# Optimization experiments

Hardware: AMD Instinct MI355X
Metric: run time of the kernel (lower is better)

The kernel has to match this reference:

```python
import jax, jax.numpy as jnp
import numpy as np

S_CONST = float(np.log(9.0))   # self.s = log(9)
K = 1.0                        # soft_sign sharpness (config.k)
RHO = 1.0
ALPHA0 = 0.01
BETA0 = 0.1
DECAY = 0.99


def soft_sign(x, k=K):
    # E2Efold soft sign: sigmoid(2*k*x)
    return jax.nn.sigmoid(2.0 * k * x)


def constraint_matrix(x):
    # x: [B, L, 4] -> m: [B, L, L]; pairing constraint AU+CG+UG outer products,
    # symmetrized, with |i-j|<=3 band zeroed (diags mask in torch version).
    base_a, base_u, base_c, base_g = x[..., 0], x[..., 1], x[..., 2], x[..., 3]

    def sym_outer(p, q):
        m = p[:, :, None] * q[:, None, :]
        return m + jnp.swapaxes(m, -1, -2)

    m = sym_outer(base_a, base_u) + sym_outer(base_c, base_g) + sym_outer(base_u, base_g)
    L = x.shape[1]
    i = jnp.arange(L)
    band = jnp.abs(i[:, None] - i[None, :]) <= 3  # [L, L] bool
    return jnp.where(band, jnp.zeros((), m.dtype), m)


def contact_a(a_hat, m):
    a = a_hat * a_hat
    a = (a + jnp.swapaxes(a, -1, -2)) * 0.5
    return a * m


def setup_inputs() -> dict:
    key = jax.random.key(0)
    k1, k2 = jax.random.split(key)
    B, L = 16, 512
    u = jax.random.normal(k1, (B, L, L), jnp.float32) * 2.0
    x = jax.random.uniform(k2, (B, L, 4), jnp.float32)
    return {"u": u, "x": x, "timesteps": 20}


def reference(u, x, timesteps):
    m = constraint_matrix(x)
    u = soft_sign(u - S_CONST) * u
    a_hat = jax.nn.sigmoid(u) * jax.lax.stop_gradient(soft_sign(u - S_CONST))
    a = contact_a(a_hat, m)
    lmbd = jax.lax.stop_gradient(jax.nn.relu(jnp.sum(a, -1) - 1.0))

    # per-step decayed learning rates: step t uses alpha0*decay^t (for grad step)
    # and alpha0*decay^(t+1) for the soft-threshold (torch decays alpha in between)
    t_idx = jnp.arange(timesteps, dtype=jnp.float32)
    alphas = ALPHA0 * DECAY ** t_idx
    betas = BETA0 * DECAY ** t_idx

    def step(carry, ab):
        lmbd, a, a_hat = carry
        alpha, beta = ab
        grad_a = -u / 2.0 + (lmbd * soft_sign(jnp.sum(a, -1) - 1.0))[..., None]
        grad = a_hat * m * (grad_a + jnp.swapaxes(grad_a, -1, -2))
        a_hat_new = a_hat - alpha * grad
        a_hat_new = jax.nn.relu(jnp.abs(a_hat_new) - RHO * alpha * DECAY)
        a_hat_new = jnp.clip(a_hat_new, -1.0, 1.0)
        a_new = contact_a(a_hat_new, m)
        lmbd_new = lmbd + beta * jax.nn.relu(jnp.sum(a_new, -1) - 1.0)
        return (lmbd_new, a_new, a_hat_new), a_new

    _, a_stack = jax.lax.scan(step, (lmbd, a, a_hat), (alphas, betas))
    return a_stack  # [timesteps, B, L, L] == a_t_list[1:]
```

## Files before the change

kernel.cpp:

```cpp
#include <hip/hip_runtime.h>
#include <math.h>

#define BB 16
#define LL 512
#define TS 20
#define TT 64
#define NT (LL / TT)
#define NPAIR (NT * (NT + 1) / 2)
#define NUNIT 32
#define NBLK (BB * NUNIT)
#define BLL (BB * LL * LL)
#define NROW (BB * LL)
#define RSPSTEP (BB * NT * LL)

#define S_CONST 2.19722457733621938f

__device__ __forceinline__ float sgm(float v) { return 1.0f / (1.0f + __expf(-v)); }
__device__ __forceinline__ float ahat_of(float up) {
  return sgm(up) * sgm(2.0f * (up - S_CONST));
}

__device__ __forceinline__ void st_agent(float* p, float v) {
  __hip_atomic_store(p, v, __ATOMIC_RELAXED, __HIP_MEMORY_SCOPE_AGENT);
}
__device__ __forceinline__ float ld_agent(const float* p) {
  return __hip_atomic_load(p, __ATOMIC_RELAXED, __HIP_MEMORY_SCOPE_AGENT);
}

__device__ __forceinline__ void bar_lds() {
  asm volatile("s_waitcnt lgkmcnt(0)" ::: "memory");
  __builtin_amdgcn_s_barrier();
  asm volatile("" ::: "memory");
}

__device__ __forceinline__ void decode_unit(int p, int& RI, int& RJ, bool& dg) {
  if (p < 28) {
    int base = 0, i = 0;
    while (p >= base + (NT - 1 - i)) { base += NT - 1 - i; ++i; }
    RI = i;
    RJ = i + 1 + (p - base);
    dg = false;
  } else {
    int g = p - 28;
    RI = 2 * g;
    RJ = 2 * g + 1;
    dg = true;
  }
}

__global__ __launch_bounds__(256, 2) void k_fused(const float* __restrict__ u,
                                                  const float* __restrict__ x,
                                                  float* __restrict__ rsp,
                                                  float* __restrict__ out) {
  __shared__ float t1[TT][TT + 1];
  __shared__ float t2[TT][TT + 1];
  __shared__ float colp1[16][TT];
  __shared__ float colp2[16][TT];
  __shared__ float rp1[TT];
  __shared__ float rp2[TT];
  __shared__ float xr[2][TT][4];
  __shared__ float xt[2][TT][4];
  __shared__ float cI[TT];
  __shared__ float cJ[TT];

  int b = blockIdx.x / NUNIT;
  int p = blockIdx.x % NUNIT;
  int RI, RJ;
  bool dg;
  decode_unit(p, RI, RJ, dg);
  int C1 = dg ? RI : RJ;
  int C2 = dg ? RJ : RI;

  int tid = threadIdx.x;
  int tx = tid & 15, ty = tid >> 4;

  if (tid < 128) {
    int which = tid >> 6;
    int r = tid & 63;
    int gi = (which ? RJ : RI) * TT + r;
    const float* xp = x + ((b * LL) + gi) * 4;
    float A = xp[0], U = xp[1], C = xp[2], G = xp[3];
    xr[which][r][0] = A; xr[which][r][1] = U; xr[which][r][2] = C; xr[which][r][3] = G;
    xt[which][r][0] = U; xt[which][r][1] = A + G; xt[which][r][2] = G; xt[which][r][3] = C + U;
  }

  int lrow = 0;
  if (tid < 128) {
    int which = tid >> 6;
    int r = tid & 63;
    lrow = (which ? RJ : RI) * TT + r;
  }
  float lmbd = 0.0f;

  float av1[4][4], av2[4][4];
  float wv1[4][4], wv2[4][4];
  float mv1[4][4], mv2[4][4];

  __syncthreads();

#pragma unroll
  for (int k = 0; k < 4; ++k) {
    int r = ty + 16 * k;
    {
      int i = RI * TT + r;
      int off = (b * LL + i) * LL + C1 * TT + 4 * tx;
      float4 u4 = *reinterpret_cast<const float4*>(u + off);
      float uu[4] = {u4.x, u4.y, u4.z, u4.w};
#pragma unroll
      for (int q = 0; q < 4; ++q) {
        float up = sgm(2.0f * (uu[q] - S_CONST)) * uu[q];
        t1[r][4 * tx + q] = up;
        av1[k][q] = ahat_of(up);
      }
    }
    {
      int i = RJ * TT + r;
      int off = (b * LL + i) * LL + C2 * TT + 4 * tx;
      float4 u4 = *reinterpret_cast<const float4*>(u + off);
      float uu[4] = {u4.x, u4.y, u4.z, u4.w};
#pragma unroll
      for (int q = 0; q < 4; ++q) {
        float up = sgm(2.0f * (uu[q] - S_CONST)) * uu[q];
        t2[r][4 * tx + q] = up;
        av2[k][q] = ahat_of(up);
      }
    }
  }
  __syncthreads();

  {
    float (*T1)[TT + 1] = dg ? t1 : t2;
    float (*T2)[TT + 1] = dg ? t2 : t1;
    float (*xc1)[4] = dg ? xt[0] : xt[1];
    float (*xc2)[4] = dg ? xt[1] : xt[0];
    float* rsp0 = rsp;

#pragma unroll
    for (int k = 0; k < 4; ++k) {
      int r = ty + 16 * k;
      {
        int i = RI * TT + r;
        float rs = 0.0f;
#pragma unroll
        for (int q = 0; q < 4; ++q) {
          int c = 4 * tx + q;
          int j = C1 * TT + c;
          float upT = T1[c][r];
          wv1[k][q] = -0.5f * (t1[r][c] + upT);
          int d = i - j; d = d < 0 ? -d : d;
          float mm = (d <= 3) ? 0.0f
                              : xr[0][r][0] * xc1[c][0] + xr[0][r][1] * xc1[c][1] +
                                    xr[0][r][2] * xc1[c][2] + xr[0][r][3] * xc1[c][3];
          mv1[k][q] = mm;
          float aT = ahat_of(upT);
          float a = av1[k][q];
          rs += 0.5f * (a * a + aT * aT) * mm;
        }
        rs += __shfl_xor(rs, 1); rs += __shfl_xor(rs, 2);
        rs += __shfl_xor(rs, 4); rs += __shfl_xor(rs, 8);
        if (tx == 0) st_agent(&rsp0[(b * NT + C1) * LL + i], rs + 1.0f);
      }
      {
        int i = RJ * TT + r;
        float rs = 0.0f;
#pragma unroll
        for (int q = 0; q < 4; ++q) {
          int c = 4 * tx + q;
          int j = C2 * TT + c;
          float upT = T2[c][r];
          wv2[k][q] = -0.5f * (t2[r][c] + upT);
          int d = i - j; d = d < 0 ? -d : d;
          float mm = (d <= 3) ? 0.0f
                              : xr[1][r][0] * xc2[c][0] + xr[1][r][1] * xc2[c][1] +
                                    xr[1][r][2] * xc2[c][2] + xr[1][r][3] * xc2[c][3];
          mv2[k][q] = mm;
          float aT = ahat_of(upT);
          float a = av2[k][q];
          rs += 0.5f * (a * a + aT * aT) * mm;
        }
        rs += __shfl_xor(rs, 1); rs += __shfl_xor(rs, 2);
        rs += __shfl_xor(rs, 4); rs += __shfl_xor(rs, 8);
        if (tx == 0) st_agent(&rsp0[(b * NT + C2) * LL + i], rs + 1.0f);
      }
    }
  }

  float (*T1)[TT + 1] = dg ? t1 : t2;
  float (*T2)[TT + 1] = dg ? t2 : t1;

  float alpha = 0.01f;
  float beta_prev = 0.0f;

  for (int t = 0; t < TS; ++t) {
    if (tid < 128) {
      const float* rp = rsp + (size_t)t * RSPSTEP + b * NT * LL + lrow;
      float v0, v1, v2, v3, v4, v5, v6, v7;
      for (;;) {
        v0 = ld_agent(rp + 0 * LL);
        v1 = ld_agent(rp + 1 * LL);
        v2 = ld_agent(rp + 2 * LL);
        v3 = ld_agent(rp + 3 * LL);
        v4 = ld_agent(rp + 4 * LL);
        v5 = ld_agent(rp + 5 * LL);
        v6 = ld_agent(rp + 6 * LL);
        v7 = ld_agent(rp + 7 * LL);
        bool ok = (v0 != 0.0f) & (v1 != 0.0f) & (v2 != 0.0f) & (v3 != 0.0f) &
                  (v4 != 0.0f) & (v5 != 0.0f) & (v6 != 0.0f) & (v7 != 0.0f);
        if (__all(ok)) break;
        __builtin_amdgcn_s_sleep(2);
        asm volatile("" ::: "memory");
      }
      float rsv = ((v0 + v1) + (v2 + v3)) + ((v4 + v5) + (v6 + v7));
      float dv = rsv - 9.0f;
      float rel = dv > 0.0f ? dv : 0.0f;
      lmbd = (t == 0) ? rel : lmbd + beta_prev * rel;
      float cv = lmbd * sgm(2.0f * dv);
      if (tid >= 64) cJ[tid & 63] = cv; else cI[tid] = cv;
    } else if (t > 0) {
      int tid2 = tid - 128;
      int tx2 = tid2 & 15, ty2 = tid2 >> 4;
      float* op = out + (size_t)(t - 1) * BLL;
#pragma unroll
      for (int k = 0; k < 8; ++k) {
        int r = ty2 + 8 * k;
        {
          int off = (b * LL + RI * TT + r) * LL + C1 * TT + 4 * tx2;
          float res[4];
#pragma unroll
          for (int q = 0; q < 4; ++q) {
            int c = 4 * tx2 + q;
            res[q] = t1[r][c] + T1[c][r];
          }
          *reinterpret_cast<float4*>(op + off) = make_float4(res[0], res[1], res[2], res[3]);
        }
        {
          int off = (b * LL + RJ * TT + r) * LL + C2 * TT + 4 * tx2;
          float res[4];
#pragma unroll
          for (int q = 0; q < 4; ++q) {
            int c = 4 * tx2 + q;
            res[q] = t2[r][c] + T2[c][r];
          }
          *reinterpret_cast<float4*>(op + off) = make_float4(res[0], res[1], res[2], res[3]);
        }
      }
    }
    bar_lds();

    float thr = alpha * 0.99f;
    float* cc1 = dg ? cI : cJ;
    float* cc2 = dg ? cJ : cI;

    float cp1[4] = {0.f, 0.f, 0.f, 0.f};
    float cp2[4] = {0.f, 0.f, 0.f, 0.f};
#pragma unroll
    for (int k = 0; k < 4; ++k) {
      int r = ty + 16 * k;
      {
        float ci = cI[r];
        float rsv = 0.0f;
#pragma unroll
        for (int q = 0; q < 4; ++q) {
          int c = 4 * tx + q;
          float a = av1[k][q];
          float g = a * mv1[k][q] * (wv1[k][q] + ci + cc1[c]);
          float an = a - alpha * g;
          an = fabsf(an) - thr;
          an = an > 0.0f ? an : 0.0f;
          an = an < 1.0f ? an : 1.0f;
          av1[k][q] = an;
          float v = 0.5f * an * an * mv1[k][q];
          t1[r][c] = v;
          rsv += v;
          cp1[q] += v;
        }
        rsv += __shfl_xor(rsv, 1); rsv += __shfl_xor(rsv, 2);
        rsv += __shfl_xor(rsv, 4); rsv += __shfl_xor(rsv, 8);
        if (tx == 0) rp1[r] = rsv;
      }
      {
        float ci = cJ[r];
        float rsv = 0.0f;
#pragma unroll
        for (int q = 0; q < 4; ++q) {
          int c = 4 * tx + q;
          float a = av2[k][q];
          float g = a * mv2[k][q] * (wv2[k][q] + ci + cc2[c]);
          float an = a - alpha * g;
          an = fabsf(an) - thr;
          an = an > 0.0f ? an : 0.0f;
          an = an < 1.0f ? an : 1.0f;
          av2[k][q] = an;
          float v = 0.5f * an * an * mv2[k][q];
          t2[r][c] = v;
          rsv += v;
          cp2[q] += v;
        }
        rsv += __shfl_xor(rsv, 1); rsv += __shfl_xor(rsv, 2);
        rsv += __shfl_xor(rsv, 4); rsv += __shfl_xor(rsv, 8);
        if (tx == 0) rp2[r] = rsv;
      }
    }
#pragma unroll
    for (int q = 0; q < 4; ++q) {
      colp1[ty][4 * tx + q] = cp1[q];
      colp2[ty][4 * tx + q] = cp2[q];
    }
    bar_lds();

    if (t < TS - 1) {
      float* rs_next = rsp + (size_t)(t + 1) * RSPSTEP;
      if (tid < 64) {
        int i = tid;
        float vsum = rp1[i];
        float (*cpA)[TT] = dg ? colp1 : colp2;
#pragma unroll
        for (int y = 0; y < 16; ++y) vsum += cpA[y][i];
        st_agent(&rs_next[(b * NT + C1) * LL + RI * TT + i], vsum + 1.0f);
      } else if (tid < 128) {
        int i = tid - 64;
        float vsum = rp2[i];
        float (*cpB)[TT] = dg ? colp2 : colp1;
#pragma unroll
        for (int y = 0; y < 16; ++y) vsum += cpB[y][i];
        st_agent(&rs_next[(b * NT + C2) * LL + RJ * TT + i], vsum + 1.0f);
      }
    }

    beta_prev = (t == 0) ? 0.1f : beta_prev * 0.99f;
    alpha *= 0.99f;
  }

  {
    float* op = out + (size_t)(TS - 1) * BLL;
#pragma unroll
    for (int k = 0; k < 4; ++k) {
      int r = ty + 16 * k;
      {
        int off = (b * LL + RI * TT + r) * LL + C1 * TT + 4 * tx;
        float res[4];
#pragma unroll
        for (int q = 0; q < 4; ++q) {
          int c = 4 * tx + q;
          res[q] = t1[r][c] + T1[c][r];
        }
        *reinterpret_cast<float4*>(op + off) = make_float4(res[0], res[1], res[2], res[3]);
      }
      {
        int off = (b * LL + RJ * TT + r) * LL + C2 * TT + 4 * tx;
        float res[4];
#pragma unroll
        for (int q = 0; q < 4; ++q) {
          int c = 4 * tx + q;
          res[q] = t2[r][c] + T2[c][r];
        }
        *reinterpret_cast<float4*>(op + off) = make_float4(res[0], res[1], res[2], res[3]);
      }
    }
  }
}

__device__ __forceinline__ void decode_pair(int p, int& I, int& J) {
  int base = 0, i = 0;
  while (p >= base + (NT - i)) { base += NT - i; ++i; }
  I = i;
  J = i + (p - base);
}

__global__ __launch_bounds__(256) void k_init(const float* __restrict__ u,
                                              const float* __restrict__ x,
                                              float* __restrict__ w,
                                              float* __restrict__ ah,
                                              float* __restrict__ rowsum) {
  __shared__ float up1[TT][TT + 1];
  __shared__ float up2[TT][TT + 1];
  __shared__ float xr[2][TT][4];
  __shared__ float xt[2][TT][4];

  int b = blockIdx.x / NPAIR;
  int p = blockIdx.x % NPAIR;
  int I, J;
  decode_pair(p, I, J);
  bool diag = (I == J);
  int tid = threadIdx.x;
  int tx = tid & 15, ty = tid >> 4;

  if (tid < 128) {
    int which = tid >> 6;
    int r = tid & 63;
    int gi = (which ? J : I) * TT + r;
    const float* xp = x + ((b * LL) + gi) * 4;
    float A = xp[0], U = xp[1], C = xp[2], G = xp[3];
    xr[which][r][0] = A; xr[which][r][1] = U; xr[which][r][2] = C; xr[which][r][3] = G;
    xt[which][r][0] = U; xt[which][r][1] = A + G; xt[which][r][2] = G; xt[which][r][3] = C + U;
  }

  float a1r[4][4], a2r[4][4];

#pragma unroll
  for (int k = 0; k < 4; ++k) {
    int r = ty + 16 * k;
    {
      int i = I * TT + r;
      int off = (b * LL + i) * LL + J * TT + 4 * tx;
      float4 u4 = *reinterpret_cast<const float4*>(u + off);
      float uu[4] = {u4.x, u4.y, u4.z, u4.w};
      float av[4];
#pragma unroll
      for (int q = 0; q < 4; ++q) {
        float up = sgm(2.0f * (uu[q] - S_CONST)) * uu[q];
        up1[r][4 * tx + q] = up;
        av[q] = ahat_of(up);
        a1r[k][q] = av[q];
      }
      *reinterpret_cast<float4*>(ah + off) = make_float4(av[0], av[1], av[2], av[3]);
    }
    if (!diag) {
      int i = J * TT + r;
      int off = (b * LL + i) * LL + I * TT + 4 * tx;
      float4 u4 = *reinterpret_cast<const float4*>(u + off);
      float uu[4] = {u4.x, u4.y, u4.z, u4.w};
      float av[4];
#pragma unroll
      for (int q = 0; q < 4; ++q) {
        float up = sgm(2.0f * (uu[q] - S_CONST)) * uu[q];
        up2[r][4 * tx + q] = up;
        av[q] = ahat_of(up);
        a2r[k][q] = av[q];
      }
      *reinterpret_cast<float4*>(ah + off) = make_float4(av[0], av[1], av[2], av[3]);
    }
  }
  __syncthreads();

  float (*U2)[TT + 1] = diag ? up1 : up2;

#pragma unroll
  for (int k = 0; k < 4; ++k) {
    int r = ty + 16 * k;
    {
      int i = I * TT + r;
      int off = (b * LL + i) * LL + J * TT + 4 * tx;
      float wv[4];
      float rs = 0.0f;
#pragma unroll
      for (int q = 0; q < 4; ++q) {
        int c = 4 * tx + q;
        int j = J * TT + c;
        float upT = U2[c][r];
        wv[q] = -0.5f * (up1[r][c] + upT);
        int d = i - j; d = d < 0 ? -d : d;
        float mm = (d <= 3) ? 0.0f
                            : xr[0][r][0] * xt[1][c][0] + xr[0][r][1] * xt[1][c][1] +
                                  xr[0][r][2] * xt[1][c][2] + xr[0][r][3] * xt[1][c][3];
        float aT = ahat_of(upT);
        float a = a1r[k][q];
        rs += 0.5f * (a * a + aT * aT) * mm;
      }
      *reinterpret_cast<float4*>(w + off) = make_float4(wv[0], wv[1], wv[2], wv[3]);
      rs += __shfl_xor(rs, 1); rs += __shfl_xor(rs, 2);
      rs += __shfl_xor(rs, 4); rs += __shfl_xor(rs, 8);
      if (tx == 0) atomicAdd(&rowsum[b * LL + i], rs);
    }
    if (!diag) {
      int i = J * TT + r;
      int off = (b * LL + i) * LL + I * TT + 4 * tx;
      float wv[4];
      float rs = 0.0f;
#pragma unroll
      for (int q = 0; q < 4; ++q) {
        int c = 4 * tx + q;
        int j = I * TT + c;
        float upT = up1[c][r];
        wv[q] = -0.5f * (up2[r][c] + upT);
        int d = i - j; d = d < 0 ? -d : d;
        float mm = (d <= 3) ? 0.0f
                            : xr[1][r][0] * xt[0][c][0] + xr[1][r][1] * xt[0][c][1] +
                                  xr[1][r][2] * xt[0][c][2] + xr[1][r][3] * xt[0][c][3];
        float aT = ahat_of(upT);
        float a = a2r[k][q];
        rs += 0.5f * (a * a + aT * aT) * mm;
      }
      *reinterpret_cast<float4*>(w + off) = make_float4(wv[0], wv[1], wv[2], wv[3]);
      rs += __shfl_xor(rs, 1); rs += __shfl_xor(rs, 2);
      rs += __shfl_xor(rs, 4); rs += __shfl_xor(rs, 8);
      if (tx == 0) atomicAdd(&rowsum[b * LL + i], rs);
    }
  }
}

__global__ __launch_bounds__(256) void k_c(float* __restrict__ lmbd,
                                           const float* __restrict__ rs,
                                           float* __restrict__ cc,
                                           float* __restrict__ rsn,
                                           float beta_prev, int first) {
  int idx = blockIdx.x * blockDim.x + threadIdx.x;
  if (idx >= NROW) return;
  float t = rs[idx] - 1.0f;
  float rel = t > 0.0f ? t : 0.0f;
  float l = first ? rel : lmbd[idx] + beta_prev * rel;
  lmbd[idx] = l;
  cc[idx] = l * sgm(2.0f * t);
  rsn[idx] = 0.0f;
}

__global__ __launch_bounds__(256) void k_step(const float* __restrict__ x,
                                              const float* __restrict__ w,
                                              float* __restrict__ ah,
                                              const float* __restrict__ cvec,
                                              float* __restrict__ rsn,
                                              float* __restrict__ out,
                                              float alpha, float thr) {
  __shared__ float an1[TT][TT + 1];
  __shared__ float an2[TT][TT + 1];
  __shared__ float xr[2][TT][4];
  __shared__ float xt[2][TT][4];
  __shared__ float cI[TT];
  __shared__ float cJ[TT];

  int b = blockIdx.x / NPAIR;
  int p = blockIdx.x % NPAIR;
  int I, J;
  decode_pair(p, I, J);
  bool diag = (I == J);
  int tid = threadIdx.x;
  int tx = tid & 15, ty = tid >> 4;

  if (tid < 128) {
    int which = tid >> 6;
    int r = tid & 63;
    int gi = (which ? J : I) * TT + r;
    const float* xp = x + ((b * LL) + gi) * 4;
    float A = xp[0], U = xp[1], C = xp[2], G = xp[3];
    xr[which][r][0] = A; xr[which][r][1] = U; xr[which][r][2] = C; xr[which][r][3] = G;
    xt[which][r][0] = U; xt[which][r][1] = A + G; xt[which][r][2] = G; xt[which][r][3] = C + U;
  } else {
    int t2i = tid - 128;
    int which = t2i >> 6;
    int r = t2i & 63;
    int gi = (which ? J : I) * TT + r;
    float cv = cvec[b * LL + gi];
    if (which) cJ[r] = cv; else cI[r] = cv;
  }
  __syncthreads();

  float m1[4][4], m2[4][4];

#pragma unroll
  for (int k = 0; k < 4; ++k) {
    int r = ty + 16 * k;
    {
      int i = I * TT + r;
      int off = (b * LL + i) * LL + J * TT + 4 * tx;
      float4 a4 = *reinterpret_cast<const float4*>(ah + off);
      float4 w4 = *reinterpret_cast<const float4*>(w + off);
      float av[4] = {a4.x, a4.y, a4.z, a4.w};
      float wv[4] = {w4.x, w4.y, w4.z, w4.w};
      float ci = cI[r];
      float res[4];
#pragma unroll
      for (int q = 0; q < 4; ++q) {
        int c = 4 * tx + q;
        int j = J * TT + c;
        int d = i - j; d = d < 0 ? -d : d;
        float mm = (d <= 3) ? 0.0f
                            : xr[0][r][0] * xt[1][c][0] + xr[0][r][1] * xt[1][c][1] +
                                  xr[0][r][2] * xt[1][c][2] + xr[0][r][3] * xt[1][c][3];
        m1[k][q] = mm;
        float g = av[q] * mm * (wv[q] + ci + cJ[c]);
        float an = av[q] - alpha * g;
        an = fabsf(an) - thr;
        an = an > 0.0f ? an : 0.0f;
        an = an < 1.0f ? an : 1.0f;
        res[q] = an;
        an1[r][c] = an;
      }
      *reinterpret_cast<float4*>(ah + off) = make_float4(res[0], res[1], res[2], res[3]);
    }
    if (!diag) {
      int i = J * TT + r;
      int off = (b * LL + i) * LL + I * TT + 4 * tx;
      float4 a4 = *reinterpret_cast<const float4*>(ah + off);
      float4 w4 = *reinterpret_cast<const float4*>(w + off);
      float av[4] = {a4.x, a4.y, a4.z, a4.w};
      float wv[4] = {w4.x, w4.y, w4.z, w4.w};
      float ci = cJ[r];
      float res[4];
#pragma unroll
      for (int q = 0; q < 4; ++q) {
        int c = 4 * tx + q;
        int j = I * TT + c;
        int d = i - j; d = d < 0 ? -d : d;
        float mm = (d <= 3) ? 0.0f
                            : xr[1][r][0] * xt[0][c][0] + xr[1][r][1] * xt[0][c][1] +
                                  xr[1][r][2] * xt[0][c][2] + xr[1][r][3] * xt[0][c][3];
        m2[k][q] = mm;
        float g = av[q] * mm * (wv[q] + ci + cI[c]);
        float an = av[q] - alpha * g;
        an = fabsf(an) - thr;
        an = an > 0.0f ? an : 0.0f;
        an = an < 1.0f ? an : 1.0f;
        res[q] = an;
        an2[r][c] = an;
      }
      *reinterpret_cast<float4*>(ah + off) = make_float4(res[0], res[1], res[2], res[3]);
    }
  }
  __syncthreads();

  float (*A2)[TT + 1] = diag ? an1 : an2;

#pragma unroll
  for (int k = 0; k < 4; ++k) {
    int r = ty + 16 * k;
    {
      int i = I * TT + r;
      int off = (b * LL + i) * LL + J * TT + 4 * tx;
      float res[4];
      float rs = 0.0f;
#pragma unroll
      for (int q = 0; q < 4; ++q) {
        int c = 4 * tx + q;
        float a = an1[r][c];
        float bt = A2[c][r];
        float v = 0.5f * (a * a + bt * bt) * m1[k][q];
        res[q] = v;
        rs += v;
      }
      *reinterpret_cast<float4*>(out + off) = make_float4(res[0], res[1], res[2], res[3]);
      rs += __shfl_xor(rs, 1); rs += __shfl_xor(rs, 2);
      rs += __shfl_xor(rs, 4); rs += __shfl_xor(rs, 8);
      if (tx == 0) atomicAdd(&rsn[b * LL + i], rs);
    }
    if (!diag) {
      int i = J * TT + r;
      int off = (b * LL + i) * LL + I * TT + 4 * tx;
      float res[4];
      float rs = 0.0f;
#pragma unroll
      for (int q = 0; q < 4; ++q) {
        int c = 4 * tx + q;
        float a = an2[r][c];
        float bt = an1[c][r];
        float v = 0.5f * (a * a + bt * bt) * m2[k][q];
        res[q] = v;
        rs += v;
      }
      *reinterpret_cast<float4*>(out + off) = make_float4(res[0], res[1], res[2], res[3]);
      rs += __shfl_xor(rs, 1); rs += __shfl_xor(rs, 2);
      rs += __shfl_xor(rs, 4); rs += __shfl_xor(rs, 8);
      if (tx == 0) atomicAdd(&rsn[b * LL + i], rs);
    }
  }
}

extern "C" void kernel_launch(void* const* d_in, const int* in_sizes, int n_in,
                              void* d_out, int out_size, void* d_ws, size_t ws_size,
                              hipStream_t stream) {
  const float* u = (const float*)d_in[0];
  const float* x = (const float*)d_in[1];
  float* out = (float*)d_out;
  float* ws = (float*)d_ws;

  float* rsp = ws;
  hipMemsetAsync(rsp, 0, (size_t)TS * RSPSTEP * sizeof(float), stream);

  void* args[] = {(void*)&u, (void*)&x, (void*)&rsp, (void*)&out};
  hipError_t err = hipLaunchCooperativeKernel((void*)k_fused, dim3(NBLK),
                                              dim3(256), args, 0, stream);
  if (err == hipSuccess) return;

  float* w = ws;
  float* ah = ws + (size_t)BLL;
  float* rsA = ws + 2 * (size_t)BLL;
  float* rsB = rsA + NROW;
  float* cc = rsB + NROW;
  float* lmbd = cc + NROW;

  hipMemsetAsync(rsA, 0, NROW * sizeof(float), stream);

  dim3 grid(BB * NPAIR);
  dim3 block(256);
  k_init<<<grid, block, 0, stream>>>(u, x, w, ah, rsA);

  float* ra = rsA;
  float* rb = rsB;
  for (int t = 0; t < TS; ++t) {
    float alpha = 0.01f * powf(0.99f, (float)t);
    float beta_prev = (t > 0) ? 0.1f * powf(0.99f, (float)(t - 1)) : 0.0f;
    k_c<<<dim3((NROW + 255) / 256), block, 0, stream>>>(lmbd, ra, cc, rb, beta_prev,
                                                        t == 0 ? 1 : 0);
    k_step<<<grid, block, 0, stream>>>(x, w, ah, cc, rb, out + (size_t)t * BLL, alpha,
                                       alpha * 0.99f);
    float* tmp = ra; ra = rb; rb = tmp;
  }
}
```

Baseline: 412.8 us.

## Move output writes after update phase, fold scale factors, use nontemporal stores

```diff
diff --git a/kernel.cpp b/kernel.cpp
--- a/kernel.cpp
+++ b/kernel.cpp
@@ -14,6 +14,8 @@
 #define RSPSTEP (BB * NT * LL)
 
 #define S_CONST 2.19722457733621938f
+
+typedef float float4n __attribute__((ext_vector_type(4)));
 
 __device__ __forceinline__ float sgm(float v) { return 1.0f / (1.0f + __expf(-v)); }
 __device__ __forceinline__ float ahat_of(float up) {
@@ -146,15 +148,16 @@
           int c = 4 * tx + q;
           int j = C1 * TT + c;
           float upT = T1[c][r];
-          wv1[k][q] = -0.5f * (t1[r][c] + upT);
+          wv1[k][q] = -(t1[r][c] + upT);
           int d = i - j; d = d < 0 ? -d : d;
           float mm = (d <= 3) ? 0.0f
                               : xr[0][r][0] * xc1[c][0] + xr[0][r][1] * xc1[c][1] +
                                     xr[0][r][2] * xc1[c][2] + xr[0][r][3] * xc1[c][3];
-          mv1[k][q] = mm;
+          float mh = 0.5f * mm;
+          mv1[k][q] = mh;
           float aT = ahat_of(upT);
           float a = av1[k][q];
-          rs += 0.5f * (a * a + aT * aT) * mm;
+          rs += (a * a + aT * aT) * mh;
         }
         rs += __shfl_xor(rs, 1); rs += __shfl_xor(rs, 2);
         rs += __shfl_xor(rs, 4); rs += __shfl_xor(rs, 8);
@@ -168,15 +171,16 @@
           int c = 4 * tx + q;
           int j = C2 * TT + c;
           float upT = T2[c][r];
-          wv2[k][q] = -0.5f * (t2[r][c] + upT);
+          wv2[k][q] = -(t2[r][c] + upT);
           int d = i - j; d = d < 0 ? -d : d;
           float mm = (d <= 3) ? 0.0f
                               : xr[1][r][0] * xc2[c][0] + xr[1][r][1] * xc2[c][1] +
                                     xr[1][r][2] * xc2[c][2] + xr[1][r][3] * xc2[c][3];
-          mv2[k][q] = mm;
+          float mh = 0.5f * mm;
+          mv2[k][q] = mh;
           float aT = ahat_of(upT);
           float a = av2[k][q];
-          rs += 0.5f * (a * a + aT * aT) * mm;
+          rs += (a * a + aT * aT) * mh;
         }
         rs += __shfl_xor(rs, 1); rs += __shfl_xor(rs, 2);
         rs += __shfl_xor(rs, 4); rs += __shfl_xor(rs, 8);
@@ -214,42 +218,21 @@
       float dv = rsv - 9.0f;
       float rel = dv > 0.0f ? dv : 0.0f;
       lmbd = (t == 0) ? rel : lmbd + beta_prev * rel;
-      float cv = lmbd * sgm(2.0f * dv);
-      if (tid >= 64) cJ[tid & 63] = cv; else cI[tid] = cv;
-    } else if (t > 0) {
-      int tid2 = tid - 128;
-      int tx2 = tid2 & 15, ty2 = tid2 >> 4;
-      float* op = out + (size_t)(t - 1) * BLL;
-#pragma unroll
-      for (int k = 0; k < 8; ++k) {
-        int r = ty2 + 8 * k;
-        {
-          int off = (b * LL + RI * TT + r) * LL + C1 * TT + 4 * tx2;
-          float res[4];
-#pragma unroll
-          for (int q = 0; q < 4; ++q) {
-            int c = 4 * tx2 + q;
-            res[q] = t1[r][c] + T1[c][r];
-          }
-          *reinterpret_cast<float4*>(op + off) = make_float4(res[0], res[1], res[2], res[3]);
-        }
-        {
-          int off = (b * LL + RJ * TT + r) * LL + C2 * TT + 4 * tx2;
-          float res[4];
-#pragma unroll
-          for (int q = 0; q < 4; ++q) {
-            int c = 4 * tx2 + q;
-            res[q] = t2[r][c] + T2[c][r];
-          }
-          *reinterpret_cast<float4*>(op + off) = make_float4(res[0], res[1], res[2], res[3]);
-        }
-      }
+      float cv2 = 2.0f * (lmbd * sgm(2.0f * dv));
+      if (tid >= 64) cJ[tid & 63] = cv2; else cI[tid] = cv2;
     }
     bar_lds();
 
     float thr = alpha * 0.99f;
     float* cc1 = dg ? cI : cJ;
     float* cc2 = dg ? cJ : cI;
+
+    float cq1[4], cq2[4];
+#pragma unroll
+    for (int q = 0; q < 4; ++q) {
+      cq1[q] = cc1[4 * tx + q];
+      cq2[q] = cc2[4 * tx + q];
+    }
 
     float cp1[4] = {0.f, 0.f, 0.f, 0.f};
     float cp2[4] = {0.f, 0.f, 0.f, 0.f};
@@ -263,13 +246,15 @@
         for (int q = 0; q < 4; ++q) {
           int c = 4 * tx + q;
           float a = av1[k][q];
-          float g = a * mv1[k][q] * (wv1[k][q] + ci + cc1[c]);
-          float an = a - alpha * g;
-          an = fabsf(an) - thr;
-          an = an > 0.0f ? an : 0.0f;
-          an = an < 1.0f ? an : 1.0f;
+          float mh = mv1[k][q];
+          float s2 = wv1[k][q] + ci + cq1[q];
+          float tt = mh * s2;
+          float sc = fmaf(-alpha, tt, 1.0f);
+          float an = a * sc;
+          float f = fabsf(an) - thr;
+          an = fminf(fmaxf(f, 0.0f), 1.0f);
           av1[k][q] = an;
-          float v = 0.5f * an * an * mv1[k][q];
+          float v = an * an * mh;
           t1[r][c] = v;
           rsv += v;
           cp1[q] += v;
@@ -285,13 +270,15 @@
         for (int q = 0; q < 4; ++q) {
           int c = 4 * tx + q;
           float a = av2[k][q];
-          float g = a * mv2[k][q] * (wv2[k][q] + ci + cc2[c]);
-          float an = a - alpha * g;
-          an = fabsf(an) - thr;
-          an = an > 0.0f ? an : 0.0f;
-          an = an < 1.0f ? an : 1.0f;
+          float mh = mv2[k][q];
+          float s2 = wv2[k][q] + ci + cq2[q];
+          float tt = mh * s2;
+          float sc = fmaf(-alpha, tt, 1.0f);
+          float an = a * sc;
+          float f = fabsf(an) - thr;
+          an = fminf(fmaxf(f, 0.0f), 1.0f);
           av2[k][q] = an;
-          float v = 0.5f * an * an * mv2[k][q];
+          float v = an * an * mh;
           t2[r][c] = v;
           rsv += v;
           cp2[q] += v;
@@ -308,55 +295,57 @@
     }
     bar_lds();
 
-    if (t < TS - 1) {
-      float* rs_next = rsp + (size_t)(t + 1) * RSPSTEP;
-      if (tid < 64) {
-        int i = tid;
-        float vsum = rp1[i];
-        float (*cpA)[TT] = dg ? colp1 : colp2;
-#pragma unroll
-        for (int y = 0; y < 16; ++y) vsum += cpA[y][i];
-        st_agent(&rs_next[(b * NT + C1) * LL + RI * TT + i], vsum + 1.0f);
-      } else if (tid < 128) {
-        int i = tid - 64;
-        float vsum = rp2[i];
-        float (*cpB)[TT] = dg ? colp2 : colp1;
-#pragma unroll
-        for (int y = 0; y < 16; ++y) vsum += cpB[y][i];
-        st_agent(&rs_next[(b * NT + C2) * LL + RJ * TT + i], vsum + 1.0f);
+    if (tid < 128) {
+      if (t < TS - 1) {
+        float* rs_next = rsp + (size_t)(t + 1) * RSPSTEP;
+        if (tid < 64) {
+          int i = tid;
+          float vsum = rp1[i];
+          float (*cpA)[TT] = dg ? colp1 : colp2;
+#pragma unroll
+          for (int y = 0; y < 16; ++y) vsum += cpA[y][i];
+          st_agent(&rs_next[(b * NT + C1) * LL + RI * TT + i], vsum + 1.0f);
+        } else {
+          int i = tid - 64;
+          float vsum = rp2[i];
+          float (*cpB)[TT] = dg ? colp2 : colp1;
+#pragma unroll
+          for (int y = 0; y < 16; ++y) vsum += cpB[y][i];
+          st_agent(&rs_next[(b * NT + C2) * LL + RJ * TT + i], vsum + 1.0f);
+        }
+      }
+    } else {
+      int tid2 = tid - 128;
+      int tx2 = tid2 & 15, ty2 = tid2 >> 4;
+      float* op = out + (size_t)t * BLL;
+#pragma unroll
+      for (int k = 0; k < 8; ++k) {
+        int r = ty2 + 8 * k;
+        {
+          int off = (b * LL + RI * TT + r) * LL + C1 * TT + 4 * tx2;
+          float4n res;
+#pragma unroll
+          for (int q = 0; q < 4; ++q) {
+            int c = 4 * tx2 + q;
+            res[q] = t1[r][c] + T1[c][r];
+          }
+          __builtin_nontemporal_store(res, reinterpret_cast<float4n*>(op + off));
+        }
+        {
+          int off = (b * LL + RJ * TT + r) * LL + C2 * TT + 4 * tx2;
+          float4n res;
+#pragma unroll
+          for (int q = 0; q < 4; ++q) {
+            int c = 4 * tx2 + q;
+            res[q] = t2[r][c] + T2[c][r];
+          }
+          __builtin_nontemporal_store(res, reinterpret_cast<float4n*>(op + off));
+        }
       }
     }
 
     beta_prev = (t == 0) ? 0.1f : beta_prev * 0.99f;
     alpha *= 0.99f;
-  }
-
-  {
-    float* op = out + (size_t)(TS - 1) * BLL;
-#pragma unroll
-    for (int k = 0; k < 4; ++k) {
-      int r = ty + 16 * k;
-      {
-        int off = (b * LL + RI * TT + r) * LL + C1 * TT + 4 * tx;
-        float res[4];
-#pragma unroll
-        for (int q = 0; q < 4; ++q) {
-          int c = 4 * tx + q;
-          res[q] = t1[r][c] + T1[c][r];
-        }
-        *reinterpret_cast<float4*>(op + off) = make_float4(res[0], res[1], res[2], res[3]);
-      }
-      {
-        int off = (b * LL + RJ * TT + r) * LL + C2 * TT + 4 * tx;
-        float res[4];
-#pragma unroll
-        for (int q = 0; q < 4; ++q) {
-          int c = 4 * tx + q;
-          res[q] = t2[r][c] + T2[c][r];
-        }
-        *reinterpret_cast<float4*>(op + off) = make_float4(res[0], res[1], res[2], res[3]);
-      }
-    }
   }
 }
 
@@ -663,7 +652,7 @@
   float* ws = (float*)d_ws;
 
   float* rsp = ws;
-  hipMemsetAsync(rsp, 0, (size_t)TS * RSPSTEP * sizeof(float), stream);
+  (void)hipMemsetAsync(rsp, 0, (size_t)TS * RSPSTEP * sizeof(float), stream);
 
   void* args[] = {(void*)&u, (void*)&x, (void*)&rsp, (void*)&out};
   hipError_t err = hipLaunchCooperativeKernel((void*)k_fused, dim3(NBLK),
@@ -677,7 +666,7 @@
   float* cc = rsB + NROW;
   float* lmbd = cc + NROW;
 
-  hipMemsetAsync(rsA, 0, NROW * sizeof(float), stream);
+  (void)hipMemsetAsync(rsA, 0, NROW * sizeof(float), stream);
 
   dim3 grid(BB * NPAIR);
   dim3 block(256);
```

New measurement: 398.6 us (median of 2 runs). 3.5% less time.
